# Kernel tuning notes

Hardware: AMD Instinct MI355X
Metric: run time of the kernel (lower is better)

Reference implementation:

```python
import jax, jax.numpy as jnp
import numpy as np

BN_EPS = 1e-5

def _maxpool2x2(t):
    # t: [B, C, H, W] -> [B, C, H//2, W//2]
    B, C, H, W = t.shape
    return t.reshape(B, C, H // 2, 2, W // 2, 2).max(axis=(3, 5))

def setup_inputs() -> dict:
    key = jax.random.key(0)
    ks = jax.random.split(key, 7)
    B, C, D, H, W = 16, 256, 128, 64, 64
    return {
        "x": jax.random.normal(ks[0], (B, C, H, W), dtype=jnp.float32),
        "g_w": jax.random.normal(ks[1], (D, C), dtype=jnp.float32) * (1.0 / np.sqrt(C)),
        "g_b": jax.random.normal(ks[2], (D,), dtype=jnp.float32) * 0.01,
        "w_w": jax.random.normal(ks[3], (C, D), dtype=jnp.float32) * (1.0 / np.sqrt(D)),
        "w_b": jax.random.normal(ks[4], (C,), dtype=jnp.float32) * 0.01,
        "gamma": jax.random.normal(ks[5], (C,), dtype=jnp.float32),
        "beta": jax.random.normal(ks[6], (C,), dtype=jnp.float32),
    }

def reference(x, g_w, g_b, w_w, w_b, gamma, beta):
    B, C, H, W = x.shape
    D = g_w.shape[0]
    # g branch: 1x1 conv C->D then 2x2 maxpool, flatten -> [B, M, D]
    g_x = jnp.einsum('bchw,dc->bdhw', x, g_w) + g_b[None, :, None, None]
    g_x = _maxpool2x2(g_x).reshape(B, D, -1).transpose(0, 2, 1)      # [B, M, D]
    # theta: raw x flattened -> [B, N, C]; phi: maxpooled x -> [B, C, M]
    theta = x.reshape(B, C, -1).transpose(0, 2, 1)                    # [B, N, C]
    phi = _maxpool2x2(x).reshape(B, C, -1)                            # [B, C, M]
    f = jnp.einsum('bnc,bcm->bnm', theta, phi)                        # [B, N, M]
    attn = jax.nn.softmax(f, axis=-1)
    y = jnp.einsum('bnm,bmd->bnd', attn, g_x)                         # [B, N, D]
    y = y.transpose(0, 2, 1).reshape(B, D, H, W)
    # W: 1x1 conv D->C then BatchNorm2d (training mode: batch stats)
    w_y = jnp.einsum('bdhw,cd->bchw', y, w_w) + w_b[None, :, None, None]
    mean = w_y.mean(axis=(0, 2, 3))
    var = w_y.var(axis=(0, 2, 3))  # biased, matching torch BN normalization
    w_y = (w_y - mean[None, :, None, None]) * jax.lax.rsqrt(var + BN_EPS)[None, :, None, None]
    w_y = w_y * gamma[None, :, None, None] + beta[None, :, None, None]
    return w_y + x
```

## Files before the change

kernel.cpp:

```cpp
#include <hip/hip_runtime.h>
#include <hip/hip_bf16.h>

typedef _Float16 half8 __attribute__((ext_vector_type(8)));
typedef float f32x4 __attribute__((ext_vector_type(4)));
typedef unsigned uint4e __attribute__((ext_vector_type(4)));
typedef unsigned uint2e __attribute__((ext_vector_type(2)));

#define B_ 16
#define C_ 256
#define D_ 128
#define H_ 64
#define W_ 64
#define N_ 4096
#define M_ 1024
#define NCH 32

static constexpr size_t WS_PHI   = 0;
static constexpr size_t WS_GPOOL = WS_PHI   + (size_t)B_*M_*C_*2;
static constexpr size_t WS_Y     = WS_GPOOL + (size_t)B_*D_*M_*2;
static constexpr size_t WS_BNSUM = WS_Y     + (size_t)B_*N_*D_*2;
static constexpr size_t WS_BNSSQ = WS_BNSUM + (size_t)C_*4;
static constexpr size_t WS_PSUM  = WS_BNSSQ + (size_t)C_*4;
static constexpr size_t WS_PSSQ  = WS_PSUM  + (size_t)1024*256*4;
static constexpr size_t WS_GW16  = WS_PSSQ  + (size_t)1024*256*4;
static constexpr size_t WS_WW16  = WS_GW16  + (size_t)D_*C_*2;

typedef __attribute__((address_space(3))) void lds_vt;
typedef const __attribute__((address_space(1))) void gbl_vt;

__device__ __forceinline__ void gl2lds16(const void* g, void* s) {
  __builtin_amdgcn_global_load_lds((gbl_vt*)g, (lds_vt*)s, 16, 0, 0);
}

__device__ __forceinline__ unsigned pkrtz(float a, float b) {
  auto v = __builtin_amdgcn_cvt_pkrtz(a, b);
  return __builtin_bit_cast(unsigned, v);
}

__device__ __forceinline__ unsigned xor32_swap(unsigned v) {
#if __has_builtin(__builtin_amdgcn_permlane32_swap)
  auto pr = __builtin_amdgcn_permlane32_swap(v, v, false, false);
  uint2e p = __builtin_bit_cast(uint2e, pr);
  return (threadIdx.x & 32) ? p[0] : p[1];
#else
  return __shfl_xor(v, 32, 64);
#endif
}
__device__ __forceinline__ float xor32f(float v) {
  return __builtin_bit_cast(float, xor32_swap(__builtin_bit_cast(unsigned, v)));
}

__global__ __launch_bounds__(256) void conv16_kernel(
    const float* __restrict__ gw, const float* __restrict__ ww,
    _Float16* __restrict__ gw16, _Float16* __restrict__ ww16) {
  const int i = blockIdx.x*256 + threadIdx.x;
  gw16[i] = (_Float16)gw[i];
  ww16[i] = (_Float16)ww[i];
}

__global__ __launch_bounds__(512, 4) void fused_pre_kernel(
    const float* __restrict__ x, const _Float16* __restrict__ gw16,
    const float* __restrict__ g_b, _Float16* __restrict__ phi,
    _Float16* __restrict__ gpool) {
  const int i = blockIdx.x;
  const int b = blockIdx.y;
  const int t = threadIdx.x;
  const int w = t >> 6, l = t & 63, gq = (l >> 4) & 3, c16 = l & 15;
  const int wn = w & 3, wd = w >> 2;

  __shared__ _Float16 x_s[256][130];

  {
    const float* xb = x + (size_t)b*C_*N_ + (size_t)i*128;
#pragma unroll
    for (int it = 0; it < 16; ++it) {
      const int id = it*512 + t;
      const int c = id >> 5, nq = id & 31;
      float4 u = *(const float4*)(xb + (size_t)c*N_ + nq*4);
      unsigned* dst = (unsigned*)&x_s[c][nq*4];
      dst[0] = pkrtz(u.x, u.y);
      dst[1] = pkrtz(u.z, u.w);
    }
  }
  __syncthreads();

  f32x4 acc[4][2];
#pragma unroll
  for (int ds = 0; ds < 4; ++ds) {
    acc[ds][0] = (f32x4){0.f,0.f,0.f,0.f};
    acc[ds][1] = (f32x4){0.f,0.f,0.f,0.f};
  }

  const int nn0 = wn*16 + c16;
  const int mrow = i*32 + wn*8 + (c16 >> 1);

  for (int kk = 0; kk < 8; ++kk) {
    const int c0 = kk*32 + gq*8;
    half8 bf0, bf1;
#pragma unroll
    for (int j = 0; j < 8; ++j) {
      bf0[j] = x_s[c0 + j][nn0];
      bf1[j] = x_s[c0 + j][nn0 + 64];
    }
    if (wd == 0) {
      half8 pk_;
#pragma unroll
      for (int j = 0; j < 8; ++j) {
        float v = fmaxf((float)bf0[j], (float)bf1[j]);
        v = fmaxf(v, __shfl_xor(v, 1, 64));
        pk_[j] = (_Float16)v;
      }
      if (!(l & 1))
        *(half8*)(phi + ((size_t)b*M_ + mrow)*C_ + c0) = pk_;
    }
#pragma unroll
    for (int ds = 0; ds < 4; ++ds) {
      half8 af = *(const half8*)(gw16 + (size_t)((wd*4 + ds)*16 + c16)*C_ + c0);
      acc[ds][0] = __builtin_amdgcn_mfma_f32_16x16x32_f16(af, bf0, acc[ds][0], 0, 0, 0);
      acc[ds][1] = __builtin_amdgcn_mfma_f32_16x16x32_f16(af, bf1, acc[ds][1], 0, 0, 0);
    }
  }

#pragma unroll
  for (int ds = 0; ds < 4; ++ds) {
#pragma unroll
    for (int r = 0; r < 4; ++r) {
      const int d = (wd*4 + ds)*16 + gq*4 + r;
      float v = fmaxf(acc[ds][0][r], acc[ds][1][r]);
      v = fmaxf(v, __shfl_xor(v, 1, 64));
      if (!(l & 1))
        gpool[((size_t)b*D_ + d)*M_ + mrow] = (_Float16)(v + g_b[d]);
    }
  }
}

__device__ __forceinline__ half8 build_pa(const float p0[4], const float p1[4], int gq) {
  unsigned d0 = pkrtz(p0[0], p0[1]);
  unsigned d1 = pkrtz(p0[2], p0[3]);
  unsigned e0 = pkrtz(p1[0], p1[1]);
  unsigned e1 = pkrtz(p1[2], p1[3]);
  unsigned D0 = __shfl_xor(d0, 16, 64), D1 = __shfl_xor(d1, 16, 64);
  unsigned E0 = __shfl_xor(e0, 16, 64), E1 = __shfl_xor(e1, 16, 64);
  const bool lo = gq < 2;
  unsigned s0 = lo ? e0 : d0, s1 = lo ? e1 : d1;
  unsigned s2 = lo ? E0 : D0, s3 = lo ? E1 : D1;
  unsigned R0 = xor32_swap(s0), R1 = xor32_swap(s1);
  unsigned R2 = xor32_swap(s2), R3 = xor32_swap(s3);
  uint4e u;
  u[0] = gq==0 ? d0 : gq==1 ? R2 : gq==2 ? R0 : E0;
  u[1] = gq==0 ? d1 : gq==1 ? R3 : gq==2 ? R1 : E1;
  u[2] = gq==0 ? D0 : gq==1 ? R0 : gq==2 ? R2 : e0;
  u[3] = gq==0 ? D1 : gq==1 ? R1 : gq==2 ? R3 : e1;
  return __builtin_bit_cast(half8, u);
}

__global__ __launch_bounds__(512, 4) void attn_kernel(
    const float* __restrict__ x, const _Float16* __restrict__ phi,
    const _Float16* __restrict__ gpool, _Float16* __restrict__ y) {
  const int nt = blockIdx.x;
  const int b  = blockIdx.y;
  const int t  = threadIdx.x;
  const int w = t >> 6, l = t & 63, gq = (l >> 4) & 3, c16 = l & 15;

  __shared__ alignas(16) _Float16 phi_s[3][32*256];
  __shared__ alignas(16) _Float16 gp_s[3][128*32];

  half8 qf[8];
  {
    const int nq = nt*128 + w*16 + c16;
#pragma unroll
    for (int kk = 0; kk < 8; ++kk) {
      const int cb = kk*32 + gq*8;
      half8 q;
#pragma unroll
      for (int j = 0; j < 8; ++j) q[j] = (_Float16)x[((size_t)b*C_ + cb + j)*N_ + nq];
      qf[kk] = q;
    }
  }

  f32x4 yacc[8];
#pragma unroll
  for (int ds = 0; ds < 8; ++ds) yacc[ds] = (f32x4){0.f,0.f,0.f,0.f};
  float m_run = -INFINITY, l_run = 0.f;

  const int lhi = l >> 5, l31 = l & 31;

  auto stage = [&](int buf, int ch2) {
    const int m0 = ch2 * 32;
#pragma unroll
    for (int jj = 0; jj < 2; ++jj) {
      const int j = w*2 + jj;
      const char* src = (const char*)phi + ((size_t)(b*M_ + m0 + l31))*512 + (2*j + lhi)*16;
      gl2lds16(src, (char*)&phi_s[buf][0] + j*1024);
    }
    {
      const char* src = (const char*)gpool + (((size_t)(b*D_ + (w&1)*64 + l))*M_ + m0)*2 + (w>>1)*16;
      gl2lds16(src, (char*)&gp_s[buf][0] + w*1024);
    }
  };

  stage(0, 0);
  stage(1, 1);

  const char* pAbase = (const char*)&phi_s[0][0] + gq*512 + c16*16;
  const char* pBbase = (const char*)&gp_s[0][0] + gq*2048 + c16*16;

  for (int ch = 0; ch < NCH; ++ch) {
    const int cur = ch % 3;
    if (ch < NCH - 1) {
      asm volatile("s_waitcnt vmcnt(3)" ::: "memory");
    } else {
      asm volatile("s_waitcnt vmcnt(0)" ::: "memory");
    }
    __builtin_amdgcn_s_barrier();
    asm volatile("" ::: "memory");

    f32x4 fS[2];
    fS[0] = (f32x4){0.f,0.f,0.f,0.f}; fS[1] = (f32x4){0.f,0.f,0.f,0.f};
    const char* pA = pAbase + cur*16384;
    __builtin_amdgcn_s_setprio(1);
#pragma unroll
    for (int kk = 0; kk < 8; ++kk) {
      half8 a0 = *(const half8*)(pA + kk*2048);
      half8 a1 = *(const half8*)(pA + kk*2048 + 256);
      fS[0] = __builtin_amdgcn_mfma_f32_16x16x32_f16(a0, qf[kk], fS[0], 0, 0, 0);
      fS[1] = __builtin_amdgcn_mfma_f32_16x16x32_f16(a1, qf[kk], fS[1], 0, 0, 0);
    }
    __builtin_amdgcn_s_setprio(0);

    float cmax = fS[0][0];
#pragma unroll
    for (int mt = 0; mt < 2; ++mt)
#pragma unroll
      for (int r = 0; r < 4; ++r) cmax = fmaxf(cmax, fS[mt][r]);
    cmax = fmaxf(cmax, __shfl_xor(cmax, 16, 64));
    cmax = fmaxf(cmax, xor32f(cmax));
    if (__any(cmax - m_run > 8.0f)) {
      const float mn = fmaxf(m_run, cmax);
      const float sc = __expf(m_run - mn);
      m_run = mn;
      l_run *= sc;
      const int sci = __float_as_int(sc);
#pragma unroll
      for (int r = 0; r < 4; ++r) {
        const float scn = __int_as_float(__builtin_amdgcn_ds_bpermute(4*(gq*4 + r), sci));
#pragma unroll
        for (int ds = 0; ds < 8; ++ds) yacc[ds][r] *= scn;
      }
    }
    float p0[4], p1[4];
    float rs = 0.f;
#pragma unroll
    for (int r = 0; r < 4; ++r) {
      p0[r] = __expf(fS[0][r] - m_run);
      p1[r] = __expf(fS[1][r] - m_run);
      rs += p0[r] + p1[r];
    }
    rs += __shfl_xor(rs, 16, 64);
    rs += xor32f(rs);
    l_run += rs;
    half8 pa = build_pa(p0, p1, gq);

    const char* pB = pBbase + cur*8192;
    __builtin_amdgcn_s_setprio(1);
#pragma unroll
    for (int ds = 0; ds < 8; ++ds) {
      half8 bv = *(const half8*)(pB + ds*256);
      yacc[ds] = __builtin_amdgcn_mfma_f32_16x16x32_f16(pa, bv, yacc[ds], 0, 0, 0);
    }
    __builtin_amdgcn_s_setprio(0);

    if (ch + 2 < NCH) stage((ch + 2) % 3, ch + 2);
  }

  {
    const float inv = 1.0f / l_run;
    const int invi = __float_as_int(inv);
#pragma unroll
    for (int r = 0; r < 4; ++r) {
      const float invn = __int_as_float(__builtin_amdgcn_ds_bpermute(4*(gq*4 + r), invi));
      const int n = nt*128 + w*16 + gq*4 + r;
      _Float16* yr = y + ((size_t)b*N_ + n)*D_ + c16;
#pragma unroll
      for (int ds = 0; ds < 8; ++ds) yr[ds*16] = (_Float16)(yacc[ds][r] * invn);
    }
  }
}

__global__ __launch_bounds__(256) void stats_partial_kernel(
    const _Float16* __restrict__ y, const _Float16* __restrict__ ww16,
    const float* __restrict__ w_b, float* __restrict__ psum,
    float* __restrict__ pssq) {
  const int nt = blockIdx.x, b = blockIdx.y, t = threadIdx.x;
  const int w = t >> 6, l = t & 63, g = l >> 4, c16 = l & 15;
  const int n0 = nt*64;

  f32x4 acc[4][4];
#pragma unroll
  for (int a = 0; a < 4; ++a)
#pragma unroll
    for (int n = 0; n < 4; ++n) acc[a][n] = (f32x4){0.f,0.f,0.f,0.f};

#pragma unroll
  for (int kk = 0; kk < 4; ++kk) {
    const int d0 = kk*32 + g*8;
    half8 af[4];
#pragma unroll
    for (int cs = 0; cs < 4; ++cs)
      af[cs] = *(const half8*)(ww16 + (size_t)(w*64 + cs*16 + c16)*D_ + d0);
#pragma unroll
    for (int ns = 0; ns < 4; ++ns) {
      const int nn = n0 + ns*16 + c16;
      half8 bf = *(const half8*)&y[((size_t)b*N_ + nn)*D_ + d0];
#pragma unroll
      for (int cs = 0; cs < 4; ++cs)
        acc[cs][ns] = __builtin_amdgcn_mfma_f32_16x16x32_f16(af[cs], bf, acc[cs][ns], 0, 0, 0);
    }
  }

  const int blk = b*64 + nt;
#pragma unroll
  for (int cs = 0; cs < 4; ++cs)
#pragma unroll
    for (int r = 0; r < 4; ++r) {
      const int c = w*64 + cs*16 + g*4 + r;
      const float wb = w_b[c];
      float s = 0.f, q = 0.f;
#pragma unroll
      for (int ns = 0; ns < 4; ++ns) {
        const float v = acc[cs][ns][r] + wb;
        s += v; q += v*v;
      }
      s += __shfl_xor(s, 1, 64); s += __shfl_xor(s, 2, 64);
      s += __shfl_xor(s, 4, 64); s += __shfl_xor(s, 8, 64);
      q += __shfl_xor(q, 1, 64); q += __shfl_xor(q, 2, 64);
      q += __shfl_xor(q, 4, 64); q += __shfl_xor(q, 8, 64);
      if (c16 == 0) {
        psum[blk*C_ + c] = s;
        pssq[blk*C_ + c] = q;
      }
    }
}

__global__ __launch_bounds__(256) void stats_reduce_kernel(
    const float* __restrict__ psum, const float* __restrict__ pssq,
    float* __restrict__ bnsum, float* __restrict__ bnssq) {
  const int t = threadIdx.x;
  const int ci = t & 31, bi = t >> 5;
  const int c = blockIdx.x*32 + ci;
  float s = 0.f, q = 0.f;
  for (int k = 0; k < 128; ++k) {
    const int row = bi + k*8;
    s += psum[row*C_ + c];
    q += pssq[row*C_ + c];
  }
  __shared__ float rs[8][32], rq[8][32];
  rs[bi][ci] = s; rq[bi][ci] = q;
  __syncthreads();
  if (bi == 0) {
    float S = 0.f, Q = 0.f;
#pragma unroll
    for (int k2 = 0; k2 < 8; ++k2) { S += rs[k2][ci]; Q += rq[k2][ci]; }
    bnsum[c] = S; bnssq[c] = Q;
  }
}

__global__ __launch_bounds__(256) void wconv_bn_kernel(
    const _Float16* __restrict__ y, const _Float16* __restrict__ ww16,
    const float* __restrict__ w_b, const float* __restrict__ bnsum,
    const float* __restrict__ bnssq, const float* __restrict__ gamma,
    const float* __restrict__ beta, const float* __restrict__ x,
    float* __restrict__ out) {
  const int nt = blockIdx.x, b = blockIdx.y, t = threadIdx.x;
  const int w = t >> 6, l = t & 63, g = l >> 4, c16 = l & 15;
  const int n0 = nt*64;

  f32x4 acc[4][4];
#pragma unroll
  for (int a = 0; a < 4; ++a)
#pragma unroll
    for (int n = 0; n < 4; ++n) acc[a][n] = (f32x4){0.f,0.f,0.f,0.f};

#pragma unroll
  for (int kk = 0; kk < 4; ++kk) {
    const int d0 = kk*32 + g*8;
    half8 af[4];
#pragma unroll
    for (int cs = 0; cs < 4; ++cs)
      af[cs] = *(const half8*)(ww16 + (size_t)(w*64 + cs*16 + c16)*D_ + d0);
#pragma unroll
    for (int ns = 0; ns < 4; ++ns) {
      const int nn = n0 + ns*16 + c16;
      half8 bf = *(const half8*)&y[((size_t)b*N_ + nn)*D_ + d0];
#pragma unroll
      for (int cs = 0; cs < 4; ++cs)
        acc[cs][ns] = __builtin_amdgcn_mfma_f32_16x16x32_f16(af[cs], bf, acc[cs][ns], 0, 0, 0);
    }
  }

  const float inv_cnt = 1.0f / (float)((size_t)B_ * N_);
#pragma unroll
  for (int cs = 0; cs < 4; ++cs) {
#pragma unroll
    for (int r = 0; r < 4; ++r) {
      const int c = w*64 + cs*16 + g*4 + r;
      const float wb  = w_b[c];
      const float mean = bnsum[c] * inv_cnt;
      const float var  = bnssq[c] * inv_cnt - mean*mean;
      const float istd = rsqrtf(var + 1e-5f);
      const float ga = gamma[c], be = beta[c];
#pragma unroll
      for (int ns = 0; ns < 4; ++ns) {
        const int n = n0 + ns*16 + c16;
        const size_t idx = ((size_t)b*C_ + c)*N_ + n;
        const float v = acc[cs][ns][r] + wb;
        out[idx] = (v - mean)*istd*ga + be + x[idx];
      }
    }
  }
}

extern "C" void kernel_launch(void* const* d_in, const int* in_sizes, int n_in,
                              void* d_out, int out_size, void* d_ws, size_t ws_size,
                              hipStream_t stream) {
  const float* x     = (const float*)d_in[0];
  const float* g_w   = (const float*)d_in[1];
  const float* g_b   = (const float*)d_in[2];
  const float* w_w   = (const float*)d_in[3];
  const float* w_b   = (const float*)d_in[4];
  const float* gamma = (const float*)d_in[5];
  const float* beta  = (const float*)d_in[6];
  float* out = (float*)d_out;

  char* ws = (char*)d_ws;
  _Float16* phi   = (_Float16*)(ws + WS_PHI);
  _Float16* gpool = (_Float16*)(ws + WS_GPOOL);
  _Float16* yb    = (_Float16*)(ws + WS_Y);
  float*    bnsum = (float*)(ws + WS_BNSUM);
  float*    bnssq = (float*)(ws + WS_BNSSQ);
  float*    psum  = (float*)(ws + WS_PSUM);
  float*    pssq  = (float*)(ws + WS_PSSQ);
  _Float16* gw16  = (_Float16*)(ws + WS_GW16);
  _Float16* ww16  = (_Float16*)(ws + WS_WW16);

  conv16_kernel<<<128, 256, 0, stream>>>(g_w, w_w, gw16, ww16);
  fused_pre_kernel<<<dim3(32, 16), 512, 0, stream>>>(x, gw16, g_b, phi, gpool);
  attn_kernel<<<dim3(32, 16), 512, 0, stream>>>(x, phi, gpool, yb);
  stats_partial_kernel<<<dim3(64, 16), 256, 0, stream>>>(yb, ww16, w_b, psum, pssq);
  stats_reduce_kernel<<<8, 256, 0, stream>>>(psum, pssq, bnsum, bnssq);
  wconv_bn_kernel<<<dim3(64, 16), 256, 0, stream>>>(yb, ww16, w_b, bnsum, bnssq, gamma, beta, x, out);
}
```

Measured before the change: 189.5 us.

## Give each attention wave two query row tiles to reuse LDS operands

The attention kernel now runs 4 waves of 256 threads instead of 8 waves of 512. Each wave processes two 16-row query tiles, so every phi and gpool fragment read from LDS feeds two MFMAs. Staging per thread doubles and the vmcnt wait is adjusted to match. This cuts LDS reads and barrier participants per unit of work, at the cost of more registers per wave (doubled accumulators and query fragments) and fewer waves to hide latency.

```diff
diff --git a/kernel.cpp b/kernel.cpp
--- a/kernel.cpp
+++ b/kernel.cpp
@@ -154,48 +154,55 @@
   return __builtin_bit_cast(half8, u);
 }
 
-__global__ __launch_bounds__(512, 4) void attn_kernel(
+__global__ __launch_bounds__(256, 2) void attn_kernel(
     const float* __restrict__ x, const _Float16* __restrict__ phi,
     const _Float16* __restrict__ gpool, _Float16* __restrict__ y) {
   const int nt = blockIdx.x;
   const int b  = blockIdx.y;
   const int t  = threadIdx.x;
   const int w = t >> 6, l = t & 63, gq = (l >> 4) & 3, c16 = l & 15;
+  const int nw = nt*128 + w*32;
 
   __shared__ alignas(16) _Float16 phi_s[3][32*256];
   __shared__ alignas(16) _Float16 gp_s[3][128*32];
 
-  half8 qf[8];
-  {
-    const int nq = nt*128 + w*16 + c16;
+  half8 qf[2][8];
+#pragma unroll
+  for (int rt = 0; rt < 2; ++rt) {
+    const int nq = nw + rt*16 + c16;
 #pragma unroll
     for (int kk = 0; kk < 8; ++kk) {
       const int cb = kk*32 + gq*8;
       half8 q;
 #pragma unroll
       for (int j = 0; j < 8; ++j) q[j] = (_Float16)x[((size_t)b*C_ + cb + j)*N_ + nq];
-      qf[kk] = q;
-    }
-  }
-
-  f32x4 yacc[8];
-#pragma unroll
-  for (int ds = 0; ds < 8; ++ds) yacc[ds] = (f32x4){0.f,0.f,0.f,0.f};
-  float m_run = -INFINITY, l_run = 0.f;
+      qf[rt][kk] = q;
+    }
+  }
+
+  f32x4 yacc[2][8];
+#pragma unroll
+  for (int rt = 0; rt < 2; ++rt)
+#pragma unroll
+    for (int ds = 0; ds < 8; ++ds) yacc[rt][ds] = (f32x4){0.f,0.f,0.f,0.f};
+  float m_run[2] = {-INFINITY, -INFINITY};
+  float l_run[2] = {0.f, 0.f};
 
   const int lhi = l >> 5, l31 = l & 31;
 
   auto stage = [&](int buf, int ch2) {
     const int m0 = ch2 * 32;
 #pragma unroll
+    for (int jj = 0; jj < 4; ++jj) {
+      const int j = w*4 + jj;
+      const char* src = (const char*)phi + ((size_t)(b*M_ + m0 + l31))*512 + (2*j + lhi)*16;
+      gl2lds16(src, (char*)&phi_s[buf][0] + j*1024);
+    }
+#pragma unroll
     for (int jj = 0; jj < 2; ++jj) {
       const int j = w*2 + jj;
-      const char* src = (const char*)phi + ((size_t)(b*M_ + m0 + l31))*512 + (2*j + lhi)*16;
-      gl2lds16(src, (char*)&phi_s[buf][0] + j*1024);
-    }
-    {
-      const char* src = (const char*)gpool + (((size_t)(b*D_ + (w&1)*64 + l))*M_ + m0)*2 + (w>>1)*16;
-      gl2lds16(src, (char*)&gp_s[buf][0] + w*1024);
+      const char* src = (const char*)gpool + (((size_t)(b*D_ + (j&1)*64 + l))*M_ + m0)*2 + (j>>1)*16;
+      gl2lds16(src, (char*)&gp_s[buf][0] + j*1024);
     }
   };
 
@@ -208,81 +215,99 @@
   for (int ch = 0; ch < NCH; ++ch) {
     const int cur = ch % 3;
     if (ch < NCH - 1) {
-      asm volatile("s_waitcnt vmcnt(3)" ::: "memory");
+      asm volatile("s_waitcnt vmcnt(6)" ::: "memory");
     } else {
       asm volatile("s_waitcnt vmcnt(0)" ::: "memory");
     }
     __builtin_amdgcn_s_barrier();
     asm volatile("" ::: "memory");
 
-    f32x4 fS[2];
-    fS[0] = (f32x4){0.f,0.f,0.f,0.f}; fS[1] = (f32x4){0.f,0.f,0.f,0.f};
+    f32x4 fS[2][2];
+    fS[0][0] = (f32x4){0.f,0.f,0.f,0.f}; fS[0][1] = (f32x4){0.f,0.f,0.f,0.f};
+    fS[1][0] = (f32x4){0.f,0.f,0.f,0.f}; fS[1][1] = (f32x4){0.f,0.f,0.f,0.f};
     const char* pA = pAbase + cur*16384;
     __builtin_amdgcn_s_setprio(1);
 #pragma unroll
     for (int kk = 0; kk < 8; ++kk) {
       half8 a0 = *(const half8*)(pA + kk*2048);
       half8 a1 = *(const half8*)(pA + kk*2048 + 256);
-      fS[0] = __builtin_amdgcn_mfma_f32_16x16x32_f16(a0, qf[kk], fS[0], 0, 0, 0);
-      fS[1] = __builtin_amdgcn_mfma_f32_16x16x32_f16(a1, qf[kk], fS[1], 0, 0, 0);
+      fS[0][0] = __builtin_amdgcn_mfma_f32_16x16x32_f16(a0, qf[0][kk], fS[0][0], 0, 0, 0);
+      fS[1][0] = __builtin_amdgcn_mfma_f32_16x16x32_f16(a0, qf[1][kk], fS[1][0], 0, 0, 0);
+      fS[0][1] = __builtin_amdgcn_mfma_f32_16x16x32_f16(a1, qf[0][kk], fS[0][1], 0, 0, 0);
+      fS[1][1] = __builtin_amdgcn_mfma_f32_16x16x32_f16(a1, qf[1][kk], fS[1][1], 0, 0, 0);
     }
     __builtin_amdgcn_s_setprio(0);
 
-    float cmax = fS[0][0];
-#pragma unroll
-    for (int mt = 0; mt < 2; ++mt)
-#pragma unroll
-      for (int r = 0; r < 4; ++r) cmax = fmaxf(cmax, fS[mt][r]);
-    cmax = fmaxf(cmax, __shfl_xor(cmax, 16, 64));
-    cmax = fmaxf(cmax, xor32f(cmax));
-    if (__any(cmax - m_run > 8.0f)) {
-      const float mn = fmaxf(m_run, cmax);
-      const float sc = __expf(m_run - mn);
-      m_run = mn;
-      l_run *= sc;
-      const int sci = __float_as_int(sc);
+    float cm[2];
+#pragma unroll
+    for (int rt = 0; rt < 2; ++rt) {
+      float cmax = fS[rt][0][0];
+#pragma unroll
+      for (int mt = 0; mt < 2; ++mt)
+#pragma unroll
+        for (int r = 0; r < 4; ++r) cmax = fmaxf(cmax, fS[rt][mt][r]);
+      cmax = fmaxf(cmax, __shfl_xor(cmax, 16, 64));
+      cmax = fmaxf(cmax, xor32f(cmax));
+      cm[rt] = cmax;
+    }
+    const float grow = fmaxf(cm[0] - m_run[0], cm[1] - m_run[1]);
+    if (__any(grow > 8.0f)) {
+#pragma unroll
+      for (int rt = 0; rt < 2; ++rt) {
+        const float mn = fmaxf(m_run[rt], cm[rt]);
+        const float sc = __expf(m_run[rt] - mn);
+        m_run[rt] = mn;
+        l_run[rt] *= sc;
+        const int sci = __float_as_int(sc);
+#pragma unroll
+        for (int r = 0; r < 4; ++r) {
+          const float scn = __int_as_float(__builtin_amdgcn_ds_bpermute(4*(gq*4 + r), sci));
+#pragma unroll
+          for (int ds = 0; ds < 8; ++ds) yacc[rt][ds][r] *= scn;
+        }
+      }
+    }
+    half8 pa[2];
+#pragma unroll
+    for (int rt = 0; rt < 2; ++rt) {
+      float p0[4], p1[4];
+      float rs = 0.f;
 #pragma unroll
       for (int r = 0; r < 4; ++r) {
-        const float scn = __int_as_float(__builtin_amdgcn_ds_bpermute(4*(gq*4 + r), sci));
-#pragma unroll
-        for (int ds = 0; ds < 8; ++ds) yacc[ds][r] *= scn;
-      }
-    }
-    float p0[4], p1[4];
-    float rs = 0.f;
-#pragma unroll
-    for (int r = 0; r < 4; ++r) {
-      p0[r] = __expf(fS[0][r] - m_run);
-      p1[r] = __expf(fS[1][r] - m_run);
-      rs += p0[r] + p1[r];
-    }
-    rs += __shfl_xor(rs, 16, 64);
-    rs += xor32f(rs);
-    l_run += rs;
-    half8 pa = build_pa(p0, p1, gq);
+        p0[r] = __expf(fS[rt][0][r] - m_run[rt]);
+        p1[r] = __expf(fS[rt][1][r] - m_run[rt]);
+        rs += p0[r] + p1[r];
+      }
+      rs += __shfl_xor(rs, 16, 64);
+      rs += xor32f(rs);
+      l_run[rt] += rs;
+      pa[rt] = build_pa(p0, p1, gq);
+    }
 
     const char* pB = pBbase + cur*8192;
     __builtin_amdgcn_s_setprio(1);
 #pragma unroll
     for (int ds = 0; ds < 8; ++ds) {
       half8 bv = *(const half8*)(pB + ds*256);
-      yacc[ds] = __builtin_amdgcn_mfma_f32_16x16x32_f16(pa, bv, yacc[ds], 0, 0, 0);
+      yacc[0][ds] = __builtin_amdgcn_mfma_f32_16x16x32_f16(pa[0], bv, yacc[0][ds], 0, 0, 0);
+      yacc[1][ds] = __builtin_amdgcn_mfma_f32_16x16x32_f16(pa[1], bv, yacc[1][ds], 0, 0, 0);
     }
     __builtin_amdgcn_s_setprio(0);
 
     if (ch + 2 < NCH) stage((ch + 2) % 3, ch + 2);
   }
 
-  {
-    const float inv = 1.0f / l_run;
+#pragma unroll
+  for (int rt = 0; rt < 2; ++rt) {
+    const float inv = 1.0f / l_run[rt];
     const int invi = __float_as_int(inv);
 #pragma unroll
     for (int r = 0; r < 4; ++r) {
       const float invn = __int_as_float(__builtin_amdgcn_ds_bpermute(4*(gq*4 + r), invi));
-      const int n = nt*128 + w*16 + gq*4 + r;
+      const int n = nw + rt*16 + gq*4 + r;
       _Float16* yr = y + ((size_t)b*N_ + n)*D_ + c16;
 #pragma unroll
-      for (int ds = 0; ds < 8; ++ds) yr[ds*16] = (_Float16)(yacc[ds][r] * invn);
+      for (int ds = 0; ds < 8; ++ds) yr[ds*16] = (_Float16)(yacc[rt][ds][r] * invn);
     }
   }
 }
@@ -445,7 +470,7 @@
 
   conv16_kernel<<<128, 256, 0, stream>>>(g_w, w_w, gw16, ww16);
   fused_pre_kernel<<<dim3(32, 16), 512, 0, stream>>>(x, gw16, g_b, phi, gpool);
-  attn_kernel<<<dim3(32, 16), 512, 0, stream>>>(x, phi, gpool, yb);
+  attn_kernel<<<dim3(32, 16), 256, 0, stream>>>(x, phi, gpool, yb);
   stats_partial_kernel<<<dim3(64, 16), 256, 0, stream>>>(yb, ww16, w_b, psum, pssq);
   stats_reduce_kernel<<<8, 256, 0, stream>>>(psum, pssq, bnsum, bnssq);
   wconv_bn_kernel<<<dim3(64, 16), 256, 0, stream>>>(yb, ww16, w_b, bnsum, bnssq, gamma, beta, x, out);
```

Measured after the change: 203.0 us. 1.07x slower.

## Switch attention kernel to 32x32x16 MFMA with 32 queries per wave

Applied to the files above, without the earlier changes.

Rewrites the attention inner loop to use 32x32x16 MFMA instructions, with each wave now handling 32 query rows instead of 16, so each block covers 256 queries and the grid is halved. The larger tiles double the reuse of each shared-memory phi/gpool load per query and simplify the P-matrix register shuffle. The cost is more registers (16 Q fragments plus four 16-wide accumulators), so launch bounds drop to 2 blocks per CU. With only 256 blocks, the GPU may be poorly filled.

```diff
diff --git a/kernel.cpp b/kernel.cpp
--- a/kernel.cpp
+++ b/kernel.cpp
@@ -3,6 +3,7 @@
 
 typedef _Float16 half8 __attribute__((ext_vector_type(8)));
 typedef float f32x4 __attribute__((ext_vector_type(4)));
+typedef float f32x16 __attribute__((ext_vector_type(16)));
 typedef unsigned uint4e __attribute__((ext_vector_type(4)));
 typedef unsigned uint2e __attribute__((ext_vector_type(2)));
 
@@ -134,56 +135,30 @@
   }
 }
 
-__device__ __forceinline__ half8 build_pa(const float p0[4], const float p1[4], int gq) {
-  unsigned d0 = pkrtz(p0[0], p0[1]);
-  unsigned d1 = pkrtz(p0[2], p0[3]);
-  unsigned e0 = pkrtz(p1[0], p1[1]);
-  unsigned e1 = pkrtz(p1[2], p1[3]);
-  unsigned D0 = __shfl_xor(d0, 16, 64), D1 = __shfl_xor(d1, 16, 64);
-  unsigned E0 = __shfl_xor(e0, 16, 64), E1 = __shfl_xor(e1, 16, 64);
-  const bool lo = gq < 2;
-  unsigned s0 = lo ? e0 : d0, s1 = lo ? e1 : d1;
-  unsigned s2 = lo ? E0 : D0, s3 = lo ? E1 : D1;
-  unsigned R0 = xor32_swap(s0), R1 = xor32_swap(s1);
-  unsigned R2 = xor32_swap(s2), R3 = xor32_swap(s3);
-  uint4e u;
-  u[0] = gq==0 ? d0 : gq==1 ? R2 : gq==2 ? R0 : E0;
-  u[1] = gq==0 ? d1 : gq==1 ? R3 : gq==2 ? R1 : E1;
-  u[2] = gq==0 ? D0 : gq==1 ? R0 : gq==2 ? R2 : e0;
-  u[3] = gq==0 ? D1 : gq==1 ? R1 : gq==2 ? R3 : e1;
-  return __builtin_bit_cast(half8, u);
-}
-
-__global__ __launch_bounds__(512, 4) void attn_kernel(
+__global__ __launch_bounds__(512, 2) void attn_kernel(
     const float* __restrict__ x, const _Float16* __restrict__ phi,
     const _Float16* __restrict__ gpool, _Float16* __restrict__ y) {
   const int nt = blockIdx.x;
   const int b  = blockIdx.y;
   const int t  = threadIdx.x;
-  const int w = t >> 6, l = t & 63, gq = (l >> 4) & 3, c16 = l & 15;
+  const int w = t >> 6, l = t & 63, l31 = l & 31, lhi = l >> 5;
+  const int nq = nt*256 + w*32 + l31;
 
   __shared__ alignas(16) _Float16 phi_s[3][32*256];
   __shared__ alignas(16) _Float16 gp_s[3][128*32];
 
-  half8 qf[8];
-  {
-    const int nq = nt*128 + w*16 + c16;
-#pragma unroll
-    for (int kk = 0; kk < 8; ++kk) {
-      const int cb = kk*32 + gq*8;
-      half8 q;
-#pragma unroll
-      for (int j = 0; j < 8; ++j) q[j] = (_Float16)x[((size_t)b*C_ + cb + j)*N_ + nq];
-      qf[kk] = q;
-    }
-  }
-
-  f32x4 yacc[8];
-#pragma unroll
-  for (int ds = 0; ds < 8; ++ds) yacc[ds] = (f32x4){0.f,0.f,0.f,0.f};
+  half8 qf[16];
+#pragma unroll
+  for (int kk = 0; kk < 16; ++kk) {
+    const int cb = kk*16 + lhi*8;
+    half8 q;
+#pragma unroll
+    for (int j = 0; j < 8; ++j) q[j] = (_Float16)x[((size_t)b*C_ + cb + j)*N_ + nq];
+    qf[kk] = q;
+  }
+
+  f32x16 yacc0 = 0.f, yacc1 = 0.f, yacc2 = 0.f, yacc3 = 0.f;
   float m_run = -INFINITY, l_run = 0.f;
-
-  const int lhi = l >> 5, l31 = l & 31;
 
   auto stage = [&](int buf, int ch2) {
     const int m0 = ch2 * 32;
@@ -202,8 +177,8 @@
   stage(0, 0);
   stage(1, 1);
 
-  const char* pAbase = (const char*)&phi_s[0][0] + gq*512 + c16*16;
-  const char* pBbase = (const char*)&gp_s[0][0] + gq*2048 + c16*16;
+  const char* pAbase = (const char*)&phi_s[0][0] + lhi*512 + l31*16;
+  const char* pBbase = (const char*)&gp_s[0][0] + lhi*2048 + l31*16;
 
   for (int ch = 0; ch < NCH; ++ch) {
     const int cur = ch % 3;
@@ -215,25 +190,19 @@
     __builtin_amdgcn_s_barrier();
     asm volatile("" ::: "memory");
 
-    f32x4 fS[2];
-    fS[0] = (f32x4){0.f,0.f,0.f,0.f}; fS[1] = (f32x4){0.f,0.f,0.f,0.f};
+    f32x16 fS = 0.f;
     const char* pA = pAbase + cur*16384;
     __builtin_amdgcn_s_setprio(1);
 #pragma unroll
-    for (int kk = 0; kk < 8; ++kk) {
-      half8 a0 = *(const half8*)(pA + kk*2048);
-      half8 a1 = *(const half8*)(pA + kk*2048 + 256);
-      fS[0] = __builtin_amdgcn_mfma_f32_16x16x32_f16(a0, qf[kk], fS[0], 0, 0, 0);
-      fS[1] = __builtin_amdgcn_mfma_f32_16x16x32_f16(a1, qf[kk], fS[1], 0, 0, 0);
+    for (int kk = 0; kk < 16; ++kk) {
+      half8 a0 = *(const half8*)(pA + kk*1024);
+      fS = __builtin_amdgcn_mfma_f32_32x32x16_f16(a0, qf[kk], fS, 0, 0, 0);
     }
     __builtin_amdgcn_s_setprio(0);
 
-    float cmax = fS[0][0];
-#pragma unroll
-    for (int mt = 0; mt < 2; ++mt)
-#pragma unroll
-      for (int r = 0; r < 4; ++r) cmax = fmaxf(cmax, fS[mt][r]);
-    cmax = fmaxf(cmax, __shfl_xor(cmax, 16, 64));
+    float cmax = fS[0];
+#pragma unroll
+    for (int i = 1; i < 16; ++i) cmax = fmaxf(cmax, fS[i]);
     cmax = fmaxf(cmax, xor32f(cmax));
     if (__any(cmax - m_run > 8.0f)) {
       const float mn = fmaxf(m_run, cmax);
@@ -242,31 +211,49 @@
       l_run *= sc;
       const int sci = __float_as_int(sc);
 #pragma unroll
-      for (int r = 0; r < 4; ++r) {
-        const float scn = __int_as_float(__builtin_amdgcn_ds_bpermute(4*(gq*4 + r), sci));
-#pragma unroll
-        for (int ds = 0; ds < 8; ++ds) yacc[ds][r] *= scn;
+      for (int i = 0; i < 16; ++i) {
+        const int qrow = (i & 3) + 8*(i >> 2) + 4*lhi;
+        const float scn = __int_as_float(__builtin_amdgcn_ds_bpermute(4*qrow, sci));
+        yacc0[i] *= scn; yacc1[i] *= scn; yacc2[i] *= scn; yacc3[i] *= scn;
       }
     }
-    float p0[4], p1[4];
+    float p[16];
     float rs = 0.f;
 #pragma unroll
-    for (int r = 0; r < 4; ++r) {
-      p0[r] = __expf(fS[0][r] - m_run);
-      p1[r] = __expf(fS[1][r] - m_run);
-      rs += p0[r] + p1[r];
-    }
-    rs += __shfl_xor(rs, 16, 64);
+    for (int i = 0; i < 16; ++i) { p[i] = __expf(fS[i] - m_run); rs += p[i]; }
     rs += xor32f(rs);
     l_run += rs;
-    half8 pa = build_pa(p0, p1, gq);
+
+    unsigned w0 = pkrtz(p[0],  p[1]),  w1 = pkrtz(p[2],  p[3]);
+    unsigned w2 = pkrtz(p[4],  p[5]),  w3 = pkrtz(p[6],  p[7]);
+    unsigned w4 = pkrtz(p[8],  p[9]),  w5 = pkrtz(p[10], p[11]);
+    unsigned w6 = pkrtz(p[12], p[13]), w7 = pkrtz(p[14], p[15]);
+    unsigned X0 = xor32_swap(w0), X1 = xor32_swap(w1);
+    unsigned X2 = xor32_swap(w2), X3 = xor32_swap(w3);
+    unsigned X4 = xor32_swap(w4), X5 = xor32_swap(w5);
+    unsigned X6 = xor32_swap(w6), X7 = xor32_swap(w7);
+    uint4e ua, ub;
+    if (lhi == 0) {
+      ua[0]=w0; ua[1]=w1; ua[2]=X0; ua[3]=X1;
+      ub[0]=w4; ub[1]=w5; ub[2]=X4; ub[3]=X5;
+    } else {
+      ua[0]=X2; ua[1]=X3; ua[2]=w2; ua[3]=w3;
+      ub[0]=X6; ub[1]=X7; ub[2]=w6; ub[3]=w7;
+    }
+    half8 pa0 = __builtin_bit_cast(half8, ua);
+    half8 pa1 = __builtin_bit_cast(half8, ub);
 
     const char* pB = pBbase + cur*8192;
     __builtin_amdgcn_s_setprio(1);
 #pragma unroll
-    for (int ds = 0; ds < 8; ++ds) {
-      half8 bv = *(const half8*)(pB + ds*256);
-      yacc[ds] = __builtin_amdgcn_mfma_f32_16x16x32_f16(pa, bv, yacc[ds], 0, 0, 0);
+    for (int dt = 0; dt < 4; ++dt) {
+      half8 bv0 = *(const half8*)(pB + dt*512);
+      half8 bv1 = *(const half8*)(pB + 4096 + dt*512);
+      f32x16 acc = dt==0 ? yacc0 : dt==1 ? yacc1 : dt==2 ? yacc2 : yacc3;
+      acc = __builtin_amdgcn_mfma_f32_32x32x16_f16(pa0, bv0, acc, 0, 0, 0);
+      acc = __builtin_amdgcn_mfma_f32_32x32x16_f16(pa1, bv1, acc, 0, 0, 0);
+      if (dt==0) yacc0 = acc; else if (dt==1) yacc1 = acc;
+      else if (dt==2) yacc2 = acc; else yacc3 = acc;
     }
     __builtin_amdgcn_s_setprio(0);
 
@@ -277,12 +264,15 @@
     const float inv = 1.0f / l_run;
     const int invi = __float_as_int(inv);
 #pragma unroll
-    for (int r = 0; r < 4; ++r) {
-      const float invn = __int_as_float(__builtin_amdgcn_ds_bpermute(4*(gq*4 + r), invi));
-      const int n = nt*128 + w*16 + gq*4 + r;
-      _Float16* yr = y + ((size_t)b*N_ + n)*D_ + c16;
-#pragma unroll
-      for (int ds = 0; ds < 8; ++ds) yr[ds*16] = (_Float16)(yacc[ds][r] * invn);
+    for (int i = 0; i < 16; ++i) {
+      const int qrow = (i & 3) + 8*(i >> 2) + 4*lhi;
+      const float invq = __int_as_float(__builtin_amdgcn_ds_bpermute(4*qrow, invi));
+      const int n = nt*256 + w*32 + qrow;
+      _Float16* yr = y + ((size_t)b*N_ + n)*D_ + l31;
+      yr[0]  = (_Float16)(yacc0[i] * invq);
+      yr[32] = (_Float16)(yacc1[i] * invq);
+      yr[64] = (_Float16)(yacc2[i] * invq);
+      yr[96] = (_Float16)(yacc3[i] * invq);
     }
   }
 }
@@ -445,7 +435,7 @@
 
   conv16_kernel<<<128, 256, 0, stream>>>(g_w, w_w, gw16, ww16);
   fused_pre_kernel<<<dim3(32, 16), 512, 0, stream>>>(x, gw16, g_b, phi, gpool);
-  attn_kernel<<<dim3(32, 16), 512, 0, stream>>>(x, phi, gpool, yb);
+  attn_kernel<<<dim3(16, 16), 512, 0, stream>>>(x, phi, gpool, yb);
   stats_partial_kernel<<<dim3(64, 16), 256, 0, stream>>>(yb, ww16, w_b, psum, pssq);
   stats_reduce_kernel<<<8, 256, 0, stream>>>(psum, pssq, bnsum, bnssq);
   wconv_bn_kernel<<<dim3(64, 16), 256, 0, stream>>>(yb, ww16, w_b, bnsum, bnssq, gamma, beta, x, out);
```

Measured after the change: 187.8 us (median of 2 runs). Within noise of the previous version (-0.9%).
